# Kernel optimization log

Hardware: AMD Instinct MI355X
Metric: run time of the kernel (lower is better)

The kernel has to match this reference:

```python
import jax, jax.numpy as jnp
import numpy as np

N = 200000   # n_nodes (multiple of 4, required by reshape)
E = 1600000  # n_edges (avg degree 8)
F = 32       # n_input_feats
H = 24       # n_hidden_feats (fixed by reshape 4*24)


def setup_inputs() -> dict:
    key = jax.random.key(0)
    ks = jax.random.split(key, 7)
    features = jax.random.normal(ks[0], (N, F), dtype=jnp.float32)
    src = jax.random.randint(ks[1], (E,), 0, N, dtype=jnp.int32)
    dst = jax.random.randint(ks[2], (E,), 0, N, dtype=jnp.int32)
    W1 = jax.random.normal(ks[3], (F, H), dtype=jnp.float32) * 0.1
    b1 = jnp.zeros((H,), dtype=jnp.float32)
    W2 = jax.random.normal(ks[4], (H, H), dtype=jnp.float32) * 0.1
    b2 = jnp.zeros((H,), dtype=jnp.float32)
    Wd = jax.random.normal(ks[5], (4 * H, 1), dtype=jnp.float32) * 0.1
    bd = jnp.zeros((1,), dtype=jnp.float32)
    return {"features": features, "src": src, "dst": dst,
            "W1": W1, "b1": b1, "W2": W2, "b2": b2, "Wd": Wd, "bd": bd}


def _graph_conv(feats, src, dst, W, b):
    """DGL GraphConv, norm='both': D_dst^{-1/2} A (D_src^{-1/2} X W) + b."""
    n = feats.shape[0]
    ones = jnp.ones(src.shape[0], dtype=feats.dtype)
    deg_out = jax.ops.segment_sum(ones, src, num_segments=n)
    deg_in = jax.ops.segment_sum(ones, dst, num_segments=n)
    norm_src = jax.lax.rsqrt(jnp.maximum(deg_out, 1.0))
    norm_dst = jax.lax.rsqrt(jnp.maximum(deg_in, 1.0))
    # weight applied before aggregation (in_feats >= out_feats path in DGL)
    x = (feats * norm_src[:, None]) @ W          # [N, H]
    msg = x[src]                                  # [E, H] gather
    agg = jax.ops.segment_sum(msg, dst, num_segments=n)  # [N, H] scatter-add
    return agg * norm_dst[:, None] + b


def reference(features, src, dst, W1, b1, W2, b2, Wd, bd):
    h = jax.nn.relu(_graph_conv(features, src, dst, W1, b1))
    h = jax.nn.relu(_graph_conv(h, src, dst, W2, b2))
    x = h.reshape(h.shape[0] // 4, 4 * H)         # [N/4, 96]
    return x @ Wd + bd                            # [N/4, 1]
```

## Files before the change

### kernel.cpp

```cpp
#include <hip/hip_runtime.h>
#include <hip/hip_fp16.h>

#define FF 32
#define HF 24
#define CAP 32
#define BSH 10
#define CHUNK 2048


__device__ __forceinline__ void encode24(const float* v, uint4& o0, uint4& o1) {
    float mx = 0.f;
#pragma unroll
    for (int j = 0; j < HF; j++) mx = fmaxf(mx, fabsf(v[j]));
    float inv = (mx > 0.f) ? 511.0f / mx : 0.f;
    float scale = mx * (1.0f / 511.0f);
    unsigned w[8] = {0u,0u,0u,0u,0u,0u,0u,0u};
#pragma unroll
    for (int j = 0; j < HF; j++) {
        int q = __float2int_rn(v[j] * inv);
        unsigned u = ((unsigned)q) & 0x3FFu;
        int bit = 10 * j, k = bit >> 5, sh = bit & 31;
        w[k] |= u << sh;
        if (sh > 22) w[k + 1] |= u >> (32 - sh);
    }
    w[7] |= ((unsigned)__half_as_ushort(__float2half(scale))) << 16;
    o0 = make_uint4(w[0], w[1], w[2], w[3]);
    o1 = make_uint4(w[4], w[5], w[6], w[7]);
}

__device__ __forceinline__ float rowscale(unsigned w7) {
    return __half2float(__ushort_as_half((unsigned short)(w7 >> 16)));
}

__device__ __forceinline__ void accum24(uint4 a, uint4 b, float es, float* h) {
    unsigned w[8] = {a.x, a.y, a.z, a.w, b.x, b.y, b.z, b.w};
#pragma unroll
    for (int j = 0; j < HF; j++) {
        int bit = 10 * j, k = bit >> 5, sh = bit & 31;
        unsigned lo = w[k] >> sh;
        unsigned hi = (sh > 22) ? (w[k + 1] << (32 - sh)) : 0u;
        int q = ((int)(((lo | hi) & 0x3FFu) << 22)) >> 22;
        h[j] += (float)q * es;
    }
}

__device__ __forceinline__ void gather16(
        const int* lst, int m, const uint4* __restrict__ x_in, float* h) {
    uint4 L0 = reinterpret_cast<const uint4*>(lst)[0];
    uint4 L1 = reinterpret_cast<const uint4*>(lst)[1];
    int m8 = (m < 8) ? m : 8;
#pragma unroll
    for (int e = 0; e < 8; e++) {
        if (e < m8) {
            int s = (e < 4) ? ((const int*)&L0)[e] : ((const int*)&L1)[e - 4];
            uint4 r0 = x_in[(size_t)s * 2];
            uint4 r1 = x_in[(size_t)s * 2 + 1];
            accum24(r0, r1, rowscale(r1.w), h);
        }
    }
    if (m > 8) {
        uint4 L2 = reinterpret_cast<const uint4*>(lst)[2];
        uint4 L3 = reinterpret_cast<const uint4*>(lst)[3];
        int m16 = (m < 16) ? m : 16;
#pragma unroll
        for (int e = 8; e < 16; e++) {
            if (e < m16) {
                int s = (e < 12) ? ((const int*)&L2)[e - 8] : ((const int*)&L3)[e - 12];
                uint4 r0 = x_in[(size_t)s * 2];
                uint4 r1 = x_in[(size_t)s * 2 + 1];
                accum24(r0, r1, rowscale(r1.w), h);
            }
        }
        for (int e = 16; e < m; e++) {
            int s = lst[e];
            uint4 r0 = x_in[(size_t)s * 2];
            uint4 r1 = x_in[(size_t)s * 2 + 1];
            accum24(r0, r1, rowscale(r1.w), h);
        }
    }
}

__global__ __launch_bounds__(256) void k_count(
        const int* __restrict__ src, const int* __restrict__ dst,
        int* __restrict__ C_dst, int* __restrict__ C_src, int E, int NB, int NBLK) {
    __shared__ int hd[256], hs[256];
    int tid = threadIdx.x, blk = blockIdx.x;
    hd[tid] = 0; hs[tid] = 0;
    __syncthreads();
    int base = blk * CHUNK;
#pragma unroll
    for (int it = 0; it < CHUNK / 256; it++) {
        int e = base + it * 256 + tid;
        if (e < E) {
            atomicAdd(&hd[dst[e] >> BSH], 1);
            atomicAdd(&hs[src[e] >> BSH], 1);
        }
    }
    __syncthreads();
    if (tid < NB) {
        C_dst[(size_t)tid * NBLK + blk] = hd[tid];
        C_src[(size_t)tid * NBLK + blk] = hs[tid];
    }
}

__global__ __launch_bounds__(256) void k_scan(
        int* __restrict__ C_dst, int* __restrict__ C_src,
        int* __restrict__ T_dst, int* __restrict__ T_src, int NB, int NBLK) {
    __shared__ int s[256];
    int tid = threadIdx.x;
    int isSrc = blockIdx.x >= NB;
    int b = isSrc ? blockIdx.x - NB : blockIdx.x;
    int* C = isSrc ? C_src : C_dst;
    int* T = isSrc ? T_src : T_dst;
    int carry = 0;
    int nCh = (NBLK + 255) / 256;
    for (int c = 0; c < nCh; c++) {
        int idx = c * 256 + tid;
        int val = (idx < NBLK) ? C[(size_t)b * NBLK + idx] : 0;
        s[tid] = val;
        __syncthreads();
        for (int o = 1; o < 256; o <<= 1) {
            int t = (tid >= o) ? s[tid - o] : 0;
            __syncthreads();
            s[tid] += t;
            __syncthreads();
        }
        int incl = s[tid];
        int tot = s[255];
        if (idx < NBLK) C[(size_t)b * NBLK + idx] = incl - val + carry;
        carry += tot;
        __syncthreads();
    }
    if (tid == 0) T[b] = carry;
}

__global__ __launch_bounds__(256) void k_base(
        const int* __restrict__ T_dst, const int* __restrict__ T_src,
        int* __restrict__ B_dst, int* __restrict__ B_src, int NB, int E) {
    __shared__ int s[256];
    int tid = threadIdx.x;
    int v = (tid < NB) ? T_dst[tid] : 0;
    s[tid] = v;
    __syncthreads();
    for (int o = 1; o < 256; o <<= 1) {
        int t = (tid >= o) ? s[tid - o] : 0;
        __syncthreads();
        s[tid] += t;
        __syncthreads();
    }
    if (tid < NB) B_dst[tid] = s[tid] - v;
    if (tid == 0) B_dst[NB] = E;
    __syncthreads();
    int v2 = (tid < NB) ? T_src[tid] : 0;
    s[tid] = v2;
    __syncthreads();
    for (int o = 1; o < 256; o <<= 1) {
        int t = (tid >= o) ? s[tid - o] : 0;
        __syncthreads();
        s[tid] += t;
        __syncthreads();
    }
    if (tid < NB) B_src[tid] = s[tid] - v2;
    if (tid == 0) B_src[NB] = E;
}

__global__ __launch_bounds__(256) void k_scatter(
        const int* __restrict__ src, const int* __restrict__ dst,
        const int* __restrict__ C_dst, const int* __restrict__ C_src,
        const int* __restrict__ B_dst, const int* __restrict__ B_src,
        unsigned* __restrict__ packed, int* __restrict__ srcOnly,
        int E, int NB, int NBLK) {
    __shared__ int cd[256], cs[256];
    int tid = threadIdx.x, blk = blockIdx.x;
    if (tid < NB) {
        cd[tid] = B_dst[tid] + C_dst[(size_t)tid * NBLK + blk];
        cs[tid] = B_src[tid] + C_src[(size_t)tid * NBLK + blk];
    }
    __syncthreads();
    int base = blk * CHUNK;
#pragma unroll
    for (int it = 0; it < CHUNK / 256; it++) {
        int e = base + it * 256 + tid;
        if (e < E) {
            int s = src[e], d = dst[e];
            int pd = atomicAdd(&cd[d >> BSH], 1);
            packed[pd] = ((unsigned)s << BSH) | (unsigned)(d & ((1 << BSH) - 1));
            int ps = atomicAdd(&cs[s >> BSH], 1);
            srcOnly[ps] = s;
        }
    }
}

__global__ __launch_bounds__(256) void k_fine(
        const unsigned* __restrict__ packed, const int* __restrict__ srcOnly,
        const int* __restrict__ B_dst, const int* __restrict__ B_src,
        int* __restrict__ cnt_in, float* __restrict__ normv, int* __restrict__ esrc,
        const float* __restrict__ feats, const float* __restrict__ W1,
        uint4* __restrict__ x1, int N, int NB) {
    __shared__ int cur[1 << BSH];
    int tid = threadIdx.x;
    if ((int)blockIdx.x < NB) {
        int b = blockIdx.x;
        for (int i = tid; i < (1 << BSH); i += 256) cur[i] = 0;
        __syncthreads();
        int ebeg = B_dst[b], eend = B_dst[b + 1];
        for (int e = ebeg + tid; e < eend; e += 256) {
            unsigned v = packed[e];
            int dl = v & ((1 << BSH) - 1);
            int s = (int)(v >> BSH);
            int slot = atomicAdd(&cur[dl], 1);
            if (slot < CAP) esrc[(size_t)((b << BSH) + dl) * CAP + slot] = s;
        }
        __syncthreads();
        for (int i = tid; i < (1 << BSH); i += 256) {
            int node = (b << BSH) + i;
            if (node < N) cnt_in[node] = cur[i];
        }
    } else {
        int b = blockIdx.x - NB;
        for (int i = tid; i < (1 << BSH); i += 256) cur[i] = 0;
        __syncthreads();
        int ebeg = B_src[b], eend = B_src[b + 1];
        for (int e = ebeg + tid; e < eend; e += 256)
            atomicAdd(&cur[srcOnly[e] & ((1 << BSH) - 1)], 1);
        __syncthreads();
        for (int i = tid; i < (1 << BSH); i += 256) {
            int node = (b << BSH) + i;
            if (node >= N) continue;
            float ns = rsqrtf(fmaxf((float)cur[i], 1.f));
            normv[node] = ns;
            float f[FF];
            const float4* fr = reinterpret_cast<const float4*>(feats + (size_t)node * FF);
#pragma unroll
            for (int q = 0; q < FF / 4; q++) {
                float4 vv = fr[q];
                f[4 * q + 0] = vv.x * ns; f[4 * q + 1] = vv.y * ns;
                f[4 * q + 2] = vv.z * ns; f[4 * q + 3] = vv.w * ns;
            }
            float acc[HF];
#pragma unroll
            for (int j = 0; j < HF; j++) acc[j] = 0.f;
#pragma unroll
            for (int k = 0; k < FF; k++) {
                float fk = f[k];
#pragma unroll
                for (int j = 0; j < HF; j++) acc[j] += fk * W1[k * HF + j];
            }
            uint4 o0, o1;
            encode24(acc, o0, o1);
            x1[(size_t)node * 2] = o0;
            x1[(size_t)node * 2 + 1] = o1;
        }
    }
}

__global__ __launch_bounds__(256) void k_agg_l2(
        const int* __restrict__ esrc, const int* __restrict__ cnt_in,
        const float* __restrict__ normv,
        const float* __restrict__ W2, const float* __restrict__ b1,
        const uint4* __restrict__ x_in, uint4* __restrict__ x_out, int N) {
    int node = blockIdx.x * 256 + threadIdx.x;
    if (node >= N) return;

    int deg = cnt_in[node];
    int m = (deg < CAP) ? deg : CAP;

    float h[HF];
#pragma unroll
    for (int j = 0; j < HF; j++) h[j] = 0.f;
    gather16(esrc + (size_t)node * CAP, m, x_in, h);

    float nd = rsqrtf(fmaxf((float)deg, 1.f));
    float nsn = normv[node];
    float t24[HF];
#pragma unroll
    for (int j = 0; j < HF; j++)
        t24[j] = fmaxf(h[j] * nd + b1[j], 0.f) * nsn;

    float o[HF];
#pragma unroll
    for (int j = 0; j < HF; j++) o[j] = 0.f;
#pragma unroll
    for (int k = 0; k < HF; k++) {
        float tk = t24[k];
#pragma unroll
        for (int j = 0; j < HF; j++) o[j] += tk * W2[k * HF + j];
    }
    uint4 o0, o1;
    encode24(o, o0, o1);
    x_out[(size_t)node * 2] = o0;
    x_out[(size_t)node * 2 + 1] = o1;
}

__global__ __launch_bounds__(256) void k_agg_fin(
        const int* __restrict__ esrc, const int* __restrict__ cnt_in,
        const float* __restrict__ Wd, const float* __restrict__ b2,
        const float* __restrict__ bd,
        const uint4* __restrict__ x_in, float* __restrict__ out, int N) {
    int node = blockIdx.x * 256 + threadIdx.x;
    bool ok = (node < N);

    float h[HF];
#pragma unroll
    for (int j = 0; j < HF; j++) h[j] = 0.f;

    int deg = 0;
    if (ok) {
        deg = cnt_in[node];
        int m = (deg < CAP) ? deg : CAP;
        gather16(esrc + (size_t)node * CAP, m, x_in, h);
    }

    float p = 0.f;
    if (ok) {
        float nd = rsqrtf(fmaxf((float)deg, 1.f));
        const float* wr = Wd + (node & 3) * HF;
#pragma unroll
        for (int j = 0; j < HF; j++)
            p += fmaxf(h[j] * nd + b2[j], 0.f) * wr[j];
    }
    p += __shfl_xor(p, 1);
    p += __shfl_xor(p, 2);
    if (ok && ((threadIdx.x & 3) == 0)) out[node >> 2] = p + bd[0];
}

extern "C" void kernel_launch(void* const* d_in, const int* in_sizes, int n_in,
                              void* d_out, int out_size, void* d_ws, size_t ws_size,
                              hipStream_t stream) {
    const float* feats = (const float*)d_in[0];
    const int* srcp = (const int*)d_in[1];
    const int* dstp = (const int*)d_in[2];
    const float* W1 = (const float*)d_in[3];
    const float* b1 = (const float*)d_in[4];
    const float* W2 = (const float*)d_in[5];
    const float* b2 = (const float*)d_in[6];
    const float* Wd = (const float*)d_in[7];
    const float* bd = (const float*)d_in[8];
    float* out = (float*)d_out;

    int N = in_sizes[0] / FF;
    int E = in_sizes[1];

    int NB = (N + (1 << BSH) - 1) >> BSH;
    int NBLK = (E + CHUNK - 1) / CHUNK;

    size_t off = 0;
    int* cnt_in = (int*)d_ws + off;                 off += (size_t)N;          off = (off + 255) & ~255ull;
    float* normv = (float*)d_ws + off;              off += (size_t)N;          off = (off + 255) & ~255ull;
    uint4* x1 = (uint4*)((int*)d_ws + off);         off += (size_t)8 * N;      off = (off + 255) & ~255ull;
    int* esrc = (int*)d_ws + off;                   off += (size_t)CAP * N;    off = (off + 255) & ~255ull;
    int* C_dst = (int*)d_ws + off;                  off += (size_t)NB * NBLK;  off = (off + 255) & ~255ull;
    int* C_src = (int*)d_ws + off;                  off += (size_t)NB * NBLK;  off = (off + 255) & ~255ull;
    int* T_dst = (int*)d_ws + off;                  off += 256;
    int* T_src = (int*)d_ws + off;                  off += 256;
    int* B_dst = (int*)d_ws + off;                  off += 256;
    int* B_src = (int*)d_ws + off;                  off += 256;
    unsigned* packed = (unsigned*)((int*)d_ws + off); size_t packedOff = off; off += (size_t)E; off = (off + 255) & ~255ull;
    int* srcOnly = (int*)d_ws + off;
    uint4* x2 = (uint4*)((int*)d_ws + packedOff);

    k_count<<<NBLK, 256, 0, stream>>>(srcp, dstp, C_dst, C_src, E, NB, NBLK);
    k_scan<<<2 * NB, 256, 0, stream>>>(C_dst, C_src, T_dst, T_src, NB, NBLK);
    k_base<<<1, 256, 0, stream>>>(T_dst, T_src, B_dst, B_src, NB, E);
    k_scatter<<<NBLK, 256, 0, stream>>>(srcp, dstp, C_dst, C_src, B_dst, B_src,
                                        packed, srcOnly, E, NB, NBLK);
    k_fine<<<2 * NB, 256, 0, stream>>>(packed, srcOnly, B_dst, B_src, cnt_in, normv,
                                       esrc, feats, W1, x1, N, NB);

    int nbNode = (N + 255) / 256;
    k_agg_l2<<<nbNode, 256, 0, stream>>>(esrc, cnt_in, normv, W2, b1, x1, x2, N);
    k_agg_fin<<<nbNode, 256, 0, stream>>>(esrc, cnt_in, Wd, b2, bd, x2, out, N);
}
```

Baseline: 226.6 us.

## Stage edge lists in LDS, drop k_base launch, wave-shuffle scans, larger chunks

```diff
diff --git a/kernel.cpp b/kernel.cpp
--- a/kernel.cpp
+++ b/kernel.cpp
@@ -5,7 +5,7 @@
 #define HF 24
 #define CAP 32
 #define BSH 10
-#define CHUNK 2048
+#define CHUNK 4096
 
 
 __device__ __forceinline__ void encode24(const float* v, uint4& o0, uint4& o1) {
@@ -44,28 +44,24 @@
     }
 }
 
-__device__ __forceinline__ void gather16(
+__device__ __forceinline__ void gather_lds(
         const int* lst, int m, const uint4* __restrict__ x_in, float* h) {
-    uint4 L0 = reinterpret_cast<const uint4*>(lst)[0];
-    uint4 L1 = reinterpret_cast<const uint4*>(lst)[1];
     int m8 = (m < 8) ? m : 8;
 #pragma unroll
     for (int e = 0; e < 8; e++) {
         if (e < m8) {
-            int s = (e < 4) ? ((const int*)&L0)[e] : ((const int*)&L1)[e - 4];
+            int s = lst[e];
             uint4 r0 = x_in[(size_t)s * 2];
             uint4 r1 = x_in[(size_t)s * 2 + 1];
             accum24(r0, r1, rowscale(r1.w), h);
         }
     }
     if (m > 8) {
-        uint4 L2 = reinterpret_cast<const uint4*>(lst)[2];
-        uint4 L3 = reinterpret_cast<const uint4*>(lst)[3];
         int m16 = (m < 16) ? m : 16;
 #pragma unroll
         for (int e = 8; e < 16; e++) {
             if (e < m16) {
-                int s = (e < 12) ? ((const int*)&L2)[e - 8] : ((const int*)&L3)[e - 12];
+                int s = lst[e];
                 uint4 r0 = x_in[(size_t)s * 2];
                 uint4 r1 = x_in[(size_t)s * 2 + 1];
                 accum24(r0, r1, rowscale(r1.w), h);
@@ -106,9 +102,9 @@
 __global__ __launch_bounds__(256) void k_scan(
         int* __restrict__ C_dst, int* __restrict__ C_src,
         int* __restrict__ T_dst, int* __restrict__ T_src, int NB, int NBLK) {
-    __shared__ int s[256];
-    int tid = threadIdx.x;
-    int isSrc = blockIdx.x >= NB;
+    __shared__ int wsum[8];
+    int tid = threadIdx.x, lane = tid & 63, wid = tid >> 6;
+    int isSrc = (int)blockIdx.x >= NB;
     int b = isSrc ? blockIdx.x - NB : blockIdx.x;
     int* C = isSrc ? C_src : C_dst;
     int* T = isSrc ? T_src : T_dst;
@@ -116,65 +112,56 @@
     int nCh = (NBLK + 255) / 256;
     for (int c = 0; c < nCh; c++) {
         int idx = c * 256 + tid;
-        int val = (idx < NBLK) ? C[(size_t)b * NBLK + idx] : 0;
-        s[tid] = val;
+        int v = (idx < NBLK) ? C[(size_t)b * NBLK + idx] : 0;
+        int x = v;
+#pragma unroll
+        for (int o = 1; o < 64; o <<= 1) {
+            int t = __shfl_up(x, o);
+            if (lane >= o) x += t;
+        }
+        if (lane == 63) wsum[wid] = x;
         __syncthreads();
-        for (int o = 1; o < 256; o <<= 1) {
-            int t = (tid >= o) ? s[tid - o] : 0;
-            __syncthreads();
-            s[tid] += t;
-            __syncthreads();
-        }
-        int incl = s[tid];
-        int tot = s[255];
-        if (idx < NBLK) C[(size_t)b * NBLK + idx] = incl - val + carry;
+        int add = 0;
+        for (int w = 0; w < wid; w++) add += wsum[w];
+        int tot = wsum[0] + wsum[1] + wsum[2] + wsum[3];
+        if (idx < NBLK) C[(size_t)b * NBLK + idx] = x - v + add + carry;
         carry += tot;
         __syncthreads();
     }
     if (tid == 0) T[b] = carry;
 }
 
-__global__ __launch_bounds__(256) void k_base(
-        const int* __restrict__ T_dst, const int* __restrict__ T_src,
-        int* __restrict__ B_dst, int* __restrict__ B_src, int NB, int E) {
-    __shared__ int s[256];
-    int tid = threadIdx.x;
-    int v = (tid < NB) ? T_dst[tid] : 0;
-    s[tid] = v;
-    __syncthreads();
-    for (int o = 1; o < 256; o <<= 1) {
-        int t = (tid >= o) ? s[tid - o] : 0;
-        __syncthreads();
-        s[tid] += t;
-        __syncthreads();
-    }
-    if (tid < NB) B_dst[tid] = s[tid] - v;
-    if (tid == 0) B_dst[NB] = E;
-    __syncthreads();
-    int v2 = (tid < NB) ? T_src[tid] : 0;
-    s[tid] = v2;
-    __syncthreads();
-    for (int o = 1; o < 256; o <<= 1) {
-        int t = (tid >= o) ? s[tid - o] : 0;
-        __syncthreads();
-        s[tid] += t;
-        __syncthreads();
-    }
-    if (tid < NB) B_src[tid] = s[tid] - v2;
-    if (tid == 0) B_src[NB] = E;
+__device__ __forceinline__ int blockExclScan(int v, int* wsum) {
+    int lane = threadIdx.x & 63, wid = threadIdx.x >> 6;
+    int x = v;
+#pragma unroll
+    for (int o = 1; o < 64; o <<= 1) {
+        int t = __shfl_up(x, o);
+        if (lane >= o) x += t;
+    }
+    if (lane == 63) wsum[wid] = x;
+    __syncthreads();
+    int add = 0;
+    for (int w = 0; w < wid; w++) add += wsum[w];
+    __syncthreads();
+    return x - v + add;
 }
 
 __global__ __launch_bounds__(256) void k_scatter(
         const int* __restrict__ src, const int* __restrict__ dst,
         const int* __restrict__ C_dst, const int* __restrict__ C_src,
-        const int* __restrict__ B_dst, const int* __restrict__ B_src,
+        const int* __restrict__ T_dst, const int* __restrict__ T_src,
         unsigned* __restrict__ packed, int* __restrict__ srcOnly,
         int E, int NB, int NBLK) {
-    __shared__ int cd[256], cs[256];
+    __shared__ int cd[256], cs[256], wsum[8];
     int tid = threadIdx.x, blk = blockIdx.x;
+    int td = (tid < NB) ? T_dst[tid] : 0;
+    int ts = (tid < NB) ? T_src[tid] : 0;
+    int based = blockExclScan(td, wsum);
+    int bases = blockExclScan(ts, wsum);
     if (tid < NB) {
-        cd[tid] = B_dst[tid] + C_dst[(size_t)tid * NBLK + blk];
-        cs[tid] = B_src[tid] + C_src[(size_t)tid * NBLK + blk];
+        cd[tid] = based + C_dst[(size_t)tid * NBLK + blk];
+        cs[tid] = bases + C_src[(size_t)tid * NBLK + blk];
     }
     __syncthreads();
     int base = blk * CHUNK;
@@ -193,17 +180,25 @@
 
 __global__ __launch_bounds__(256) void k_fine(
         const unsigned* __restrict__ packed, const int* __restrict__ srcOnly,
-        const int* __restrict__ B_dst, const int* __restrict__ B_src,
+        const int* __restrict__ T_dst, const int* __restrict__ T_src,
         int* __restrict__ cnt_in, float* __restrict__ normv, int* __restrict__ esrc,
         const float* __restrict__ feats, const float* __restrict__ W1,
         uint4* __restrict__ x1, int N, int NB) {
     __shared__ int cur[1 << BSH];
+    __shared__ int wsum[8];
+    __shared__ int ebr[2];
     int tid = threadIdx.x;
-    if ((int)blockIdx.x < NB) {
-        int b = blockIdx.x;
-        for (int i = tid; i < (1 << BSH); i += 256) cur[i] = 0;
-        __syncthreads();
-        int ebeg = B_dst[b], eend = B_dst[b + 1];
+    int isSrc = (int)blockIdx.x >= NB;
+    int b = isSrc ? blockIdx.x - NB : blockIdx.x;
+    const int* T = isSrc ? T_src : T_dst;
+    int tv = (tid < NB) ? T[tid] : 0;
+    int excl = blockExclScan(tv, wsum);
+    if (tid == b) { ebr[0] = excl; ebr[1] = excl + tv; }
+    for (int i = tid; i < (1 << BSH); i += 256) cur[i] = 0;
+    __syncthreads();
+    int ebeg = ebr[0], eend = ebr[1];
+
+    if (!isSrc) {
         for (int e = ebeg + tid; e < eend; e += 256) {
             unsigned v = packed[e];
             int dl = v & ((1 << BSH) - 1);
@@ -217,10 +212,6 @@
             if (node < N) cnt_in[node] = cur[i];
         }
     } else {
-        int b = blockIdx.x - NB;
-        for (int i = tid; i < (1 << BSH); i += 256) cur[i] = 0;
-        __syncthreads();
-        int ebeg = B_src[b], eend = B_src[b + 1];
         for (int e = ebeg + tid; e < eend; e += 256)
             atomicAdd(&cur[srcOnly[e] & ((1 << BSH) - 1)], 1);
         __syncthreads();
@@ -259,7 +250,21 @@
         const float* __restrict__ normv,
         const float* __restrict__ W2, const float* __restrict__ b1,
         const uint4* __restrict__ x_in, uint4* __restrict__ x_out, int N) {
-    int node = blockIdx.x * 256 + threadIdx.x;
+    __shared__ int ll[256 * 33];
+    int tid = threadIdx.x;
+    int nodeBase = blockIdx.x * 256;
+    const uint4* g = reinterpret_cast<const uint4*>(esrc + (size_t)nodeBase * CAP);
+#pragma unroll
+    for (int it = 0; it < 8; it++) {
+        int idx = it * 256 + tid;
+        int t = idx >> 3, q = idx & 7;
+        uint4 v = g[idx];
+        int o = t * 33 + q * 4;
+        ll[o] = v.x; ll[o + 1] = v.y; ll[o + 2] = v.z; ll[o + 3] = v.w;
+    }
+    __syncthreads();
+
+    int node = nodeBase + tid;
     if (node >= N) return;
 
     int deg = cnt_in[node];
@@ -268,7 +273,7 @@
     float h[HF];
 #pragma unroll
     for (int j = 0; j < HF; j++) h[j] = 0.f;
-    gather16(esrc + (size_t)node * CAP, m, x_in, h);
+    gather_lds(&ll[tid * 33], m, x_in, h);
 
     float nd = rsqrtf(fmaxf((float)deg, 1.f));
     float nsn = normv[node];
@@ -297,7 +302,21 @@
         const float* __restrict__ Wd, const float* __restrict__ b2,
         const float* __restrict__ bd,
         const uint4* __restrict__ x_in, float* __restrict__ out, int N) {
-    int node = blockIdx.x * 256 + threadIdx.x;
+    __shared__ int ll[256 * 33];
+    int tid = threadIdx.x;
+    int nodeBase = blockIdx.x * 256;
+    const uint4* g = reinterpret_cast<const uint4*>(esrc + (size_t)nodeBase * CAP);
+#pragma unroll
+    for (int it = 0; it < 8; it++) {
+        int idx = it * 256 + tid;
+        int t = idx >> 3, q = idx & 7;
+        uint4 v = g[idx];
+        int o = t * 33 + q * 4;
+        ll[o] = v.x; ll[o + 1] = v.y; ll[o + 2] = v.z; ll[o + 3] = v.w;
+    }
+    __syncthreads();
+
+    int node = nodeBase + tid;
     bool ok = (node < N);
 
     float h[HF];
@@ -308,7 +327,7 @@
     if (ok) {
         deg = cnt_in[node];
         int m = (deg < CAP) ? deg : CAP;
-        gather16(esrc + (size_t)node * CAP, m, x_in, h);
+        gather_lds(&ll[tid * 33], m, x_in, h);
     }
 
     float p = 0.f;
@@ -321,7 +340,7 @@
     }
     p += __shfl_xor(p, 1);
     p += __shfl_xor(p, 2);
-    if (ok && ((threadIdx.x & 3) == 0)) out[node >> 2] = p + bd[0];
+    if (ok && ((tid & 3) == 0)) out[node >> 2] = p + bd[0];
 }
 
 extern "C" void kernel_launch(void* const* d_in, const int* in_sizes, int n_in,
@@ -348,26 +367,23 @@
     int* cnt_in = (int*)d_ws + off;                 off += (size_t)N;          off = (off + 255) & ~255ull;
     float* normv = (float*)d_ws + off;              off += (size_t)N;          off = (off + 255) & ~255ull;
     uint4* x1 = (uint4*)((int*)d_ws + off);         off += (size_t)8 * N;      off = (off + 255) & ~255ull;
-    int* esrc = (int*)d_ws + off;                   off += (size_t)CAP * N;    off = (off + 255) & ~255ull;
+    int* esrc = (int*)d_ws + off;                   off += (size_t)CAP * N + 8192; off = (off + 255) & ~255ull;
     int* C_dst = (int*)d_ws + off;                  off += (size_t)NB * NBLK;  off = (off + 255) & ~255ull;
     int* C_src = (int*)d_ws + off;                  off += (size_t)NB * NBLK;  off = (off + 255) & ~255ull;
     int* T_dst = (int*)d_ws + off;                  off += 256;
     int* T_src = (int*)d_ws + off;                  off += 256;
-    int* B_dst = (int*)d_ws + off;                  off += 256;
-    int* B_src = (int*)d_ws + off;                  off += 256;
     unsigned* packed = (unsigned*)((int*)d_ws + off); size_t packedOff = off; off += (size_t)E; off = (off + 255) & ~255ull;
     int* srcOnly = (int*)d_ws + off;
     uint4* x2 = (uint4*)((int*)d_ws + packedOff);
 
     k_count<<<NBLK, 256, 0, stream>>>(srcp, dstp, C_dst, C_src, E, NB, NBLK);
     k_scan<<<2 * NB, 256, 0, stream>>>(C_dst, C_src, T_dst, T_src, NB, NBLK);
-    k_base<<<1, 256, 0, stream>>>(T_dst, T_src, B_dst, B_src, NB, E);
-    k_scatter<<<NBLK, 256, 0, stream>>>(srcp, dstp, C_dst, C_src, B_dst, B_src,
+    k_scatter<<<NBLK, 256, 0, stream>>>(srcp, dstp, C_dst, C_src, T_dst, T_src,
                                         packed, srcOnly, E, NB, NBLK);
-    k_fine<<<2 * NB, 256, 0, stream>>>(packed, srcOnly, B_dst, B_src, cnt_in, normv,
+    k_fine<<<2 * NB, 256, 0, stream>>>(packed, srcOnly, T_dst, T_src, cnt_in, normv,
                                        esrc, feats, W1, x1, N, NB);
 
-    int nbNode = (N + 255) / 256;
-    k_agg_l2<<<nbNode, 256, 0, stream>>>(esrc, cnt_in, normv, W2, b1, x1, x2, N);
-    k_agg_fin<<<nbNode, 256, 0, stream>>>(esrc, cnt_in, Wd, b2, bd, x2, out, N);
-}
+    int nbAgg = (N + 255) / 256;
+    k_agg_l2<<<nbAgg, 256, 0, stream>>>(esrc, cnt_in, normv, W2, b1, x1, x2, N);
+    k_agg_fin<<<nbAgg, 256, 0, stream>>>(esrc, cnt_in, Wd, b2, bd, x2, out, N);
+}
```

Result: faster. 210.0 us (-7.3%).
